# Optimization experiments

Hardware: AMD Instinct MI355X
Metric: run time of the kernel (lower is better)

## Reference

```python
import jax, jax.numpy as jnp
import numpy as np

CROP = 96      # fixed GT box size (xmax-xmin == ymax-ymin == CROP)
WIN = 11       # pytorch-msssim default gaussian window
SIGMA = 1.5
DATA_RANGE = 255.0


def _gauss1d():
    c = jnp.arange(WIN, dtype=jnp.float32) - (WIN - 1) / 2.0
    g = jnp.exp(-(c * c) / (2.0 * SIGMA * SIGMA))
    return g / g.sum()


def _gfilter(x, g):
    # x: [N,C,H,W]; separable per-channel gaussian blur, VALID padding
    C = x.shape[1]
    kh = jnp.tile(g.reshape(1, 1, WIN, 1), (C, 1, 1, 1))
    kw = jnp.tile(g.reshape(1, 1, 1, WIN), (C, 1, 1, 1))
    x = jax.lax.conv_general_dilated(x, kh, (1, 1), 'VALID', feature_group_count=C)
    x = jax.lax.conv_general_dilated(x, kw, (1, 1), 'VALID', feature_group_count=C)
    return x


def _ssim_per_sample(a, b):
    # a, b: [N,C,H,W] in [0, 255]; returns [N] ssim (size_average over C,H,W)
    K1, K2 = 0.01, 0.03
    C1 = (K1 * DATA_RANGE) ** 2
    C2 = (K2 * DATA_RANGE) ** 2
    g = _gauss1d()
    mu1 = _gfilter(a, g)
    mu2 = _gfilter(b, g)
    mu1_sq, mu2_sq, mu12 = mu1 * mu1, mu2 * mu2, mu1 * mu2
    s1 = _gfilter(a * a, g) - mu1_sq
    s2 = _gfilter(b * b, g) - mu2_sq
    s12 = _gfilter(a * b, g) - mu12
    m = ((2.0 * mu12 + C1) * (2.0 * s12 + C2)) / ((mu1_sq + mu2_sq + C1) * (s1 + s2 + C2))
    return m.mean(axis=(1, 2, 3))


def _crop_all(img, ymin, xmin):
    # img: [3,H,W]; fixed-size dynamic crops -> [N,3,CROP,CROP]
    def one(y, x):
        return jax.lax.dynamic_slice(img, (0, y, x), (img.shape[0], CROP, CROP))
    return jax.vmap(one)(ymin, xmin)


def setup_inputs() -> dict:
    key = jax.random.key(0)
    k1, k2, k3, k4 = jax.random.split(key, 4)
    H, W, N = 1080, 1920, 256
    image = jax.random.uniform(k1, (3, H, W), jnp.float32) * 255.0
    image_rewrite = jnp.clip(image + jax.random.normal(k2, (3, H, W), jnp.float32) * 8.0, 0.0, 255.0)
    xmin = jax.random.randint(k3, (N,), 0, W - CROP)
    ymin = jax.random.randint(k4, (N,), 0, H - CROP)
    cls = jnp.zeros((N,), jnp.int32)
    target = jnp.stack([xmin, ymin, xmin + CROP, ymin + CROP, cls], axis=1).astype(jnp.int32)
    return {"image": image, "image_rewrite": image_rewrite, "target": target}


def reference(image, image_rewrite, target):
    xmin = target[:, 0]
    ymin = target[:, 1]
    crops = _crop_all(image, ymin, xmin)
    crops_rw = _crop_all(image_rewrite, ymin, xmin)
    ssim_vals = _ssim_per_sample(crops, crops_rw)          # [N]
    return jnp.mean(1.0 - ssim_vals) * 5.0                 # scalar loss
```

## Files before the change

kernel.cpp:

```cpp
#include <hip/hip_runtime.h>
#include <math.h>

#define CROP 96
#define WIN 11
#define OUT 86
#define IMH 1080
#define IMW 1920
#define NIT 11
#define RSW 352
#define NSLOT 32

typedef float v2f __attribute__((ext_vector_type(2)));


__global__ __launch_bounds__(256) void ssim_kernel(
    const float* __restrict__ img,
    const float* __restrict__ imgr,
    const int* __restrict__ target,
    float* __restrict__ block_sums)
{
    __shared__ __align__(16) float hbuf[NSLOT * RSW];
    __shared__ float red[256];

    const int blk = blockIdx.x;
    const int s   = blk / 3;
    const int c   = blk % 3;

    const int xmin = target[s * 5 + 0];
    const int ymin = target[s * 5 + 1];

    const size_t cbase = (size_t)c * (IMH * IMW) + (size_t)ymin * IMW + (size_t)xmin;
    const float* __restrict__ pa = img  + cbase;
    const float* __restrict__ pb = imgr + cbase;

    const int tid = threadIdx.x;

    float gw[WIN];
    {
        float sum = 0.f;
        #pragma unroll
        for (int k = 0; k < WIN; ++k) {
            const float cc = (float)k - (float)(WIN - 1) * 0.5f;
            gw[k] = expf(-(cc * cc) / (2.0f * 1.5f * 1.5f));
            sum += gw[k];
        }
        const float inv = 1.0f / sum;
        #pragma unroll
        for (int k = 0; k < WIN; ++k) gw[k] *= inv;
    }

    auto doA_task = [&](int row, int g) {
        const int xo = (g == 7) ? 74 : 12 * g;
        const float* __restrict__ ra = pa + (size_t)row * IMW + xo;
        const float* __restrict__ rb = pb + (size_t)row * IMW + xo;

        v2f aPQ[12] = {}; v2f aP2[12] = {};
        #pragma unroll
        for (int tt = 0; tt < 22; ++tt) {
            const float a = ra[tt];
            const float b = rb[tt];
            const v2f pq  = {a + b, a - b};
            const v2f pq2 = pq * pq;
            #pragma unroll
            for (int jj = 0; jj < 12; ++jj) {
                const int kk = tt - jj;
                if (kk >= 0 && kk < WIN) {
                    aPQ[jj] += pq  * gw[kk];
                    aP2[jj] += pq2 * gw[kk];
                }
            }
        }
        const int sbase = (row & (NSLOT - 1)) * RSW;
        #pragma unroll
        for (int jj = 0; jj < 12; ++jj) {
            const int x = xo + jj;
            *(float4*)&hbuf[sbase + x * 4] =
                make_float4(aPQ[jj].x, aPQ[jj].y, aP2[jj].x, aP2[jj].y);
        }
    };

    if (tid < 144) doA_task(tid >> 3, tid & 7);
    __syncthreads();

    const float C1 = 6.5025f;
    const float C2 = 58.5225f;
    float acc = 0.f;

    const int bx   = (tid < 172) ? (tid % 86) : 0;
    const int bgrp = (tid < 172) ? (tid / 86) : 0;
    const int au   = tid - 192;
    const int arow0 = (au >> 3) + 18;
    const int ag    = au & 7;

    for (int k = 0; k < NIT; ++k) {
        const int r0out = 8 * k;

        if (tid < 172) {
            const int r0 = r0out + bgrp * 4;
            v2f mPQ[4] = {}; v2f mP2[4] = {};
            #pragma unroll
            for (int tt = 0; tt < 14; ++tt) {
                const int slot = (r0 + tt) & (NSLOT - 1);
                const float4 f = *(const float4*)&hbuf[slot * RSW + bx * 4];
                const v2f fPQ = {f.x, f.y};
                const v2f fP2 = {f.z, f.w};
                #pragma unroll
                for (int jj = 0; jj < 4; ++jj) {
                    const int kk = tt - jj;
                    if (kk >= 0 && kk < WIN) {
                        mPQ[jj] += fPQ * gw[kk];
                        mP2[jj] += fP2 * gw[kk];
                    }
                }
            }
            #pragma unroll
            for (int jj = 0; jj < 4; ++jj) {
                if (r0 + jj < OUT) {
                    const v2f sq = mPQ[jj] * mPQ[jj];
                    const float mu12x2  = (sq.x - sq.y) * 0.5f;
                    const float musqsum = (sq.x + sq.y) * 0.5f;
                    const float e_dif = (mP2[jj].x - mP2[jj].y) * 0.5f;
                    const float e_sum = (mP2[jj].x + mP2[jj].y) * 0.5f;
                    const float s12x2 = e_dif - mu12x2;
                    const float ssum  = e_sum - musqsum;
                    const float num = (mu12x2 + C1) * (s12x2 + C2);
                    const float den = (musqsum + C1) * (ssum + C2);
                    acc += num * __builtin_amdgcn_rcpf(den);
                }
            }
        } else if (tid >= 192) {
            const int row = r0out + arow0;
            if (row < CROP) doA_task(row, ag);
        }
        __syncthreads();
    }

    red[tid] = acc;
    __syncthreads();
    #pragma unroll
    for (int off = 128; off > 0; off >>= 1) {
        if (tid < off) red[tid] += red[tid + off];
        __syncthreads();
    }
    if (tid == 0) block_sums[blk] = red[0];
}

__global__ __launch_bounds__(256) void ssim_finalize_kernel(
    const float* __restrict__ block_sums,
    float* __restrict__ out,
    int nblk,
    float inv_npix)
{
    __shared__ float red[256];
    const int tid = threadIdx.x;
    float s = 0.f;
    for (int i = tid; i < nblk; i += 256) s += block_sums[i];
    red[tid] = s;
    __syncthreads();
    #pragma unroll
    for (int off = 128; off > 0; off >>= 1) {
        if (tid < off) red[tid] += red[tid + off];
        __syncthreads();
    }
    if (tid == 0) {
        const float mean = red[0] * inv_npix;
        out[0] = 5.0f * (1.0f - mean);
    }
}

extern "C" void kernel_launch(void* const* d_in, const int* in_sizes, int n_in,
                              void* d_out, int out_size, void* d_ws, size_t ws_size,
                              hipStream_t stream)
{
    const float* img  = (const float*)d_in[0];
    const float* imgr = (const float*)d_in[1];
    const int*   tgt  = (const int*)d_in[2];
    const int N = in_sizes[2] / 5;
    const int nblk = 3 * N;

    float* block_sums = (float*)d_ws;
    const float inv_npix = 1.0f / ((float)nblk * (float)(OUT * OUT));

    ssim_kernel<<<nblk, 256, 0, stream>>>(img, imgr, tgt, block_sums);
    ssim_finalize_kernel<<<1, 256, 0, stream>>>(block_sums, (float*)d_out, nblk, inv_npix);
}
```

Baseline: 34.17 us.

## Fuse final reduction via last-block atomic, pad LDS rows, preload row loads

Replaces the separate finalize kernel with a last-block-done pattern: each block writes its partial sum, takes a ticket from an atomic counter, and the final block reduces all partials and writes the loss. The counter is cleared with a memset on the stream. This also pads the shared-memory row stride to reduce bank conflicts, sets a minimum-occupancy hint in the launch bounds, and loads each row's 22 inputs into registers before the FMA loop. The memset adds its own launch, which may offset the saved finalize launch, and the occupancy hint could force register spills.

```diff
diff --git a/kernel.cpp b/kernel.cpp
--- a/kernel.cpp
+++ b/kernel.cpp
@@ -7,20 +7,25 @@
 #define IMH 1080
 #define IMW 1920
 #define NIT 11
-#define RSW 352
+#define RSW 356
 #define NSLOT 32
 
 typedef float v2f __attribute__((ext_vector_type(2)));
 
 
-__global__ __launch_bounds__(256) void ssim_kernel(
+__global__ __launch_bounds__(256, 4) void ssim_kernel(
     const float* __restrict__ img,
     const float* __restrict__ imgr,
     const int* __restrict__ target,
-    float* __restrict__ block_sums)
+    float* __restrict__ block_sums,
+    unsigned int* __restrict__ counter,
+    float* __restrict__ out,
+    int nblk,
+    float inv_npix)
 {
     __shared__ __align__(16) float hbuf[NSLOT * RSW];
     __shared__ float red[256];
+    __shared__ unsigned int isLast;
 
     const int blk = blockIdx.x;
     const int s   = blk / 3;
@@ -54,12 +59,16 @@
         const float* __restrict__ ra = pa + (size_t)row * IMW + xo;
         const float* __restrict__ rb = pb + (size_t)row * IMW + xo;
 
+        float wa[22], wb[22];
+        #pragma unroll
+        for (int tt = 0; tt < 22; ++tt) wa[tt] = ra[tt];
+        #pragma unroll
+        for (int tt = 0; tt < 22; ++tt) wb[tt] = rb[tt];
+
         v2f aPQ[12] = {}; v2f aP2[12] = {};
         #pragma unroll
         for (int tt = 0; tt < 22; ++tt) {
-            const float a = ra[tt];
-            const float b = rb[tt];
-            const v2f pq  = {a + b, a - b};
+            const v2f pq  = {wa[tt] + wb[tt], wa[tt] - wb[tt]};
             const v2f pq2 = pq * pq;
             #pragma unroll
             for (int jj = 0; jj < 12; ++jj) {
@@ -86,9 +95,9 @@
     const float C2 = 58.5225f;
     float acc = 0.f;
 
-    const int bx   = (tid < 172) ? (tid % 86) : 0;
-    const int bgrp = (tid < 172) ? (tid / 86) : 0;
-    const int au   = tid - 192;
+    const int bx    = (tid < 172) ? (tid % 86) : 0;
+    const int bgrp  = (tid < 172) ? (tid / 86) : 0;
+    const int au    = tid - 192;
     const int arow0 = (au >> 3) + 18;
     const int ag    = au & 7;
 
@@ -142,29 +151,26 @@
         if (tid < off) red[tid] += red[tid + off];
         __syncthreads();
     }
-    if (tid == 0) block_sums[blk] = red[0];
-}
 
-__global__ __launch_bounds__(256) void ssim_finalize_kernel(
-    const float* __restrict__ block_sums,
-    float* __restrict__ out,
-    int nblk,
-    float inv_npix)
-{
-    __shared__ float red[256];
-    const int tid = threadIdx.x;
-    float s = 0.f;
-    for (int i = tid; i < nblk; i += 256) s += block_sums[i];
-    red[tid] = s;
+    if (tid == 0) {
+        block_sums[blk] = red[0];
+        __threadfence();
+        const unsigned int t = atomicAdd(counter, 1u);
+        isLast = (t == (unsigned int)(nblk - 1)) ? 1u : 0u;
+    }
     __syncthreads();
-    #pragma unroll
-    for (int off = 128; off > 0; off >>= 1) {
-        if (tid < off) red[tid] += red[tid + off];
+    if (isLast) {
+        __threadfence();
+        float ssum = 0.f;
+        for (int i = tid; i < nblk; i += 256) ssum += block_sums[i];
+        red[tid] = ssum;
         __syncthreads();
-    }
-    if (tid == 0) {
-        const float mean = red[0] * inv_npix;
-        out[0] = 5.0f * (1.0f - mean);
+        #pragma unroll
+        for (int off = 128; off > 0; off >>= 1) {
+            if (tid < off) red[tid] += red[tid + off];
+            __syncthreads();
+        }
+        if (tid == 0) out[0] = 5.0f * (1.0f - red[0] * inv_npix);
     }
 }
 
@@ -178,9 +184,12 @@
     const int N = in_sizes[2] / 5;
     const int nblk = 3 * N;
 
-    float* block_sums = (float*)d_ws;
+    float*        block_sums = (float*)d_ws;
+    unsigned int* counter    = (unsigned int*)((float*)d_ws + nblk);
+
     const float inv_npix = 1.0f / ((float)nblk * (float)(OUT * OUT));
 
-    ssim_kernel<<<nblk, 256, 0, stream>>>(img, imgr, tgt, block_sums);
-    ssim_finalize_kernel<<<1, 256, 0, stream>>>(block_sums, (float*)d_out, nblk, inv_npix);
+    hipMemsetAsync((void*)counter, 0, sizeof(unsigned int), stream);
+    ssim_kernel<<<nblk, 256, 0, stream>>>(img, imgr, tgt, block_sums, counter,
+                                          (float*)d_out, nblk, inv_npix);
 }
```

New measurement: 54.09 us. +58.3%, slower.
